# Performance work log

Hardware: AMD Instinct MI355X
Metric: run time of the kernel (lower is better)

The kernel has to match this reference:

```python
import jax, jax.numpy as jnp
import numpy as np

N = 100000
E = 1600000
IN_DIM = 128
HID = 64
NCOMM = 32


def setup_inputs() -> dict:
    key = jax.random.key(0)
    k = jax.random.split(key, 8)
    x = jax.random.normal(k[0], (N, IN_DIM), dtype=jnp.float32)
    edge_index = jax.random.randint(k[1], (2, E), 0, N, dtype=jnp.int64)
    s1 = 1.0 / np.sqrt(IN_DIM)
    s2 = 1.0 / np.sqrt(HID)
    W1 = jax.random.uniform(k[2], (IN_DIM, HID), jnp.float32, -s1, s1)
    b1 = jnp.zeros((HID,), jnp.float32)
    W2 = jax.random.uniform(k[3], (HID, HID), jnp.float32, -s2, s2)
    b2 = jnp.zeros((HID,), jnp.float32)
    Wfc = jax.random.uniform(k[4], (HID, NCOMM), jnp.float32, -s2, s2)
    bfc = jax.random.uniform(k[5], (NCOMM,), jnp.float32, -s2, s2)
    return {"x": x, "edge_index": edge_index, "W1": W1, "b1": b1,
            "W2": W2, "b2": b2, "Wfc": Wfc, "bfc": bfc}


def gcn_conv(x, row, col, norm, W, b):
    # PyG GCNConv: linear -> gather(source) * norm -> scatter_add(target) -> + bias
    h = x @ W                                    # [N, out]
    msgs = h[row] * norm[:, None]                # [E+N, out] gather (memory-bound)
    agg = jax.ops.segment_sum(msgs, col, num_segments=x.shape[0])
    return agg + b


def reference(x, edge_index, W1, b1, W2, b2, Wfc, bfc):
    n = x.shape[0]
    # add self-loops (PyG GCNConv default)
    loop = jnp.arange(n, dtype=edge_index.dtype)
    row = jnp.concatenate([edge_index[0], loop])  # source
    col = jnp.concatenate([edge_index[1], loop])  # target
    # symmetric normalization D^{-1/2} (A+I) D^{-1/2}
    deg = jax.ops.segment_sum(jnp.ones_like(col, dtype=x.dtype), col, num_segments=n)
    dinv = jnp.where(deg > 0, jax.lax.rsqrt(deg), 0.0)
    norm = dinv[row] * dinv[col]
    h = jax.nn.relu(gcn_conv(x, row, col, norm, W1, b1))   # dropout = identity (eval)
    h = jax.nn.relu(gcn_conv(h, row, col, norm, W2, b2))
    return jax.nn.sigmoid(h @ Wfc + bfc)
```

## Files before the change

kernel.cpp:

```cpp
#include <hip/hip_runtime.h>
#include <hip/hip_fp16.h>
#include <math.h>

#define N_NODES 100000
#define N_EDGES 1600000
#define IN_DIM  128
#define HID     64
#define NCOMM   32
#define NB        391
#define BSHIFT    8
#define BCAP      6144
#define EPB       4096
#define NBIN_BLK  391

typedef _Float16 f16x8 __attribute__((ext_vector_type(8)));
typedef float    f32x4 __attribute__((ext_vector_type(4)));

__global__ void k_detect(const unsigned int* __restrict__ e, int* __restrict__ flag) {
  int lane = threadIdx.x;
  unsigned v = 0;
  #pragma unroll
  for (int i = 0; i < 4; ++i) v |= e[2 * (lane * 4 + i) + 1];
  unsigned long long nz = __ballot(v != 0u);
  if (lane == 0) *flag = (nz == 0ull) ? 1 : 0;
}

__device__ __forceinline__ int load_idx(const int* e32, long long pos, int is64) {
  if (is64) return (int)(((const long long*)e32)[pos]);
  return e32[pos];
}

__global__ __launch_bounds__(256) void k_bin(const int* __restrict__ e, int* __restrict__ bcnt,
                                             unsigned* __restrict__ ebuf, const int* __restrict__ flag) {
  __shared__ int cnt[NB];
  __shared__ int base[NB];
  for (int i = threadIdx.x; i < NB; i += 256) cnt[i] = 0;
  __syncthreads();
  int is64 = *flag;
  long long eb = (long long)blockIdx.x * EPB;
  int rr[EPB / 256], cc[EPB / 256], lr[EPB / 256];
  #pragma unroll
  for (int j = 0; j < EPB / 256; ++j) {
    long long eid = eb + j * 256 + threadIdx.x;
    if (eid < N_EDGES) {
      rr[j] = load_idx(e, eid, is64);
      cc[j] = load_idx(e, (long long)N_EDGES + eid, is64);
      lr[j] = atomicAdd(&cnt[cc[j] >> BSHIFT], 1);
    }
  }
  __syncthreads();
  for (int b = threadIdx.x; b < NB; b += 256)
    base[b] = cnt[b] ? atomicAdd(&bcnt[b], cnt[b]) : 0;
  __syncthreads();
  #pragma unroll
  for (int j = 0; j < EPB / 256; ++j) {
    long long eid = eb + j * 256 + threadIdx.x;
    if (eid < N_EDGES) {
      int bb = cc[j] >> BSHIFT;
      int pos = bb * BCAP + base[bb] + lr[j];
      ebuf[pos] = ((unsigned)(cc[j] & 255) << 17) | (unsigned)rr[j];
    }
  }
}

__global__ __launch_bounds__(256) void k_degsort(const unsigned* __restrict__ ebuf, const int* __restrict__ bcnt,
                                                 float* __restrict__ dinv, int2* __restrict__ parr,
                                                 int* __restrict__ srow) {
  __shared__ int cnt[256];
  __shared__ int scn[256];
  __shared__ int cur[256];
  __shared__ unsigned eds[BCAP];
  int t = threadIdx.x;
  int b = blockIdx.x;
  int c0 = b << BSHIFT;
  int n = bcnt[b];
  cnt[t] = 0;
  __syncthreads();
  for (int i = t; i < n; i += 256) {
    unsigned w = ebuf[b * BCAP + i];
    eds[i] = w;
    atomicAdd(&cnt[w >> 17], 1);
  }
  __syncthreads();
  int d = cnt[t];
  scn[t] = d;
  __syncthreads();
  for (int off = 1; off < 256; off <<= 1) {
    int u = (t >= off) ? scn[t - off] : 0;
    __syncthreads();
    scn[t] += u;
    __syncthreads();
  }
  int sabs = b * BCAP + scn[t] - d;
  int node = c0 + t;
  if (node < N_NODES) {
    dinv[node] = rsqrtf((float)d + 1.0f);
    parr[node] = make_int2(sabs, sabs + d);
  }
  cur[t] = sabs;
  __syncthreads();
  for (int i = t; i < n; i += 256) {
    unsigned w = eds[i];
    int pos = atomicAdd(&cur[w >> 17], 1);
    srow[pos] = (int)(w & 0x1FFFFu);
  }
}

template<int K, int M, bool FINAL, bool INH>
__global__ __launch_bounds__(256) void k_mfma(const void* __restrict__ X, const float* __restrict__ W,
                                              void* __restrict__ Y, const float* __restrict__ bias,
                                              const float* __restrict__ dscale) {
  constexpr int NN = M / 16;
  constexpr int KS = K / 32;
  __shared__ char smem[M * K * 2];

  const int tid = threadIdx.x;
  for (int i = tid; i < K * M / 4; i += 256) {
    int k  = i / (M / 4);
    int mf = (i % (M / 4)) * 4;
    float4 wv = *(const float4*)(W + (size_t)k * M + mf);
    float wa[4] = {wv.x, wv.y, wv.z, wv.w};
    #pragma unroll
    for (int c = 0; c < 4; ++c) {
      int m = mf + c;
      int byte_off = m * (2 * K) + ((((k >> 3) << 4)) ^ ((m & 7) << 4)) + (k & 7) * 2;
      *(_Float16*)(smem + byte_off) = (_Float16)wa[c];
    }
  }
  __syncthreads();

  const int lane = tid & 63;
  const int wv_  = tid >> 6;
  const int rowbase = blockIdx.x * 128 + wv_ * 32;
  const int lr = lane & 15;
  const int kg = lane >> 4;
  const int r0 = rowbase + lr;
  const int r1 = r0 + 16;
  const int rc0 = (r0 < N_NODES) ? r0 : (N_NODES - 1);
  const int rc1 = (r1 < N_NODES) ? r1 : (N_NODES - 1);

  f32x4 acc[2][NN] = {};

  #pragma unroll
  for (int ks = 0; ks < KS; ++ks) {
    const int k0 = ks * 32 + kg * 8;
    f16x8 a0, a1;
    if constexpr (!INH) {
      const float* xr = (const float*)X;
      float4 u0 = *(const float4*)(xr + (size_t)rc0 * K + k0);
      float4 u1 = *(const float4*)(xr + (size_t)rc0 * K + k0 + 4);
      float4 u2 = *(const float4*)(xr + (size_t)rc1 * K + k0);
      float4 u3 = *(const float4*)(xr + (size_t)rc1 * K + k0 + 4);
      a0[0] = (_Float16)u0.x; a0[1] = (_Float16)u0.y; a0[2] = (_Float16)u0.z; a0[3] = (_Float16)u0.w;
      a0[4] = (_Float16)u1.x; a0[5] = (_Float16)u1.y; a0[6] = (_Float16)u1.z; a0[7] = (_Float16)u1.w;
      a1[0] = (_Float16)u2.x; a1[1] = (_Float16)u2.y; a1[2] = (_Float16)u2.z; a1[3] = (_Float16)u2.w;
      a1[4] = (_Float16)u3.x; a1[5] = (_Float16)u3.y; a1[6] = (_Float16)u3.z; a1[7] = (_Float16)u3.w;
    } else {
      const char* xb = (const char*)X;
      a0 = *(const f16x8*)(xb + (size_t)rc0 * (2 * K) + k0 * 2);
      a1 = *(const f16x8*)(xb + (size_t)rc1 * (2 * K) + k0 * 2);
    }
    const int slot = (k0 >> 3) << 4;
    #pragma unroll
    for (int n = 0; n < NN; ++n) {
      const int col = n * 16 + lr;
      f16x8 b = *(const f16x8*)(smem + col * (2 * K) + (slot ^ ((col & 7) << 4)));
      acc[0][n] = __builtin_amdgcn_mfma_f32_16x16x32_f16(a0, b, acc[0][n], 0, 0, 0);
      acc[1][n] = __builtin_amdgcn_mfma_f32_16x16x32_f16(a1, b, acc[1][n], 0, 0, 0);
    }
  }

  #pragma unroll
  for (int m2 = 0; m2 < 2; ++m2) {
    #pragma unroll
    for (int r = 0; r < 4; ++r) {
      const int row = rowbase + m2 * 16 + kg * 4 + r;
      if (row < N_NODES) {
        float ds = FINAL ? 0.f : dscale[row];
        #pragma unroll
        for (int n = 0; n < NN; ++n) {
          const int col = n * 16 + lr;
          float v = acc[m2][n][r];
          if constexpr (FINAL) {
            v += bias[col];
            v = 1.f / (1.f + __expf(-v));
            ((float*)Y)[(size_t)row * M + col] = v;
          } else {
            ((__half*)Y)[(size_t)row * M + col] = __float2half(v * ds);
          }
        }
      }
    }
  }
}

__device__ __forceinline__ void addrow(float* acc, uint4 h) {
  __half2 p0 = *(__half2*)&h.x;
  __half2 p1 = *(__half2*)&h.y;
  __half2 p2 = *(__half2*)&h.z;
  __half2 p3 = *(__half2*)&h.w;
  float2 f0 = __half22float2(p0);
  float2 f1 = __half22float2(p1);
  float2 f2 = __half22float2(p2);
  float2 f3 = __half22float2(p3);
  acc[0] += f0.x; acc[1] += f0.y;
  acc[2] += f1.x; acc[3] += f1.y;
  acc[4] += f2.x; acc[5] += f2.y;
  acc[6] += f3.x; acc[7] += f3.y;
}

__global__ __launch_bounds__(256) void k_agg(const __half* __restrict__ H, __half* __restrict__ O,
                                             const int2* __restrict__ parr, const int* __restrict__ srow,
                                             const float* __restrict__ dinv, const float* __restrict__ bias) {
  int wid  = (blockIdx.x * 256 + threadIdx.x) >> 6;
  int lane = threadIdx.x & 63;
  if (wid >= N_NODES) return;
  const int q  = lane >> 3;
  const int fl = lane & 7;
  const char* Hb = (const char*)H;
  int2 se = parr[wid];
  int s = se.x, e = se.y;
  float acc[8] = {0.f, 0.f, 0.f, 0.f, 0.f, 0.f, 0.f, 0.f};
  for (int j = s; j < e; j += 16) {
    int i0 = j + q;
    int i1 = j + 8 + q;
    int r0 = srow[i0];
    int r1 = srow[i1];
    r0 = (i0 < e) ? r0 : N_NODES;
    r1 = (i1 < e) ? r1 : N_NODES;
    uint4 h0 = *(const uint4*)(Hb + (size_t)((unsigned)r0 * 128u + (unsigned)fl * 16u));
    uint4 h1 = *(const uint4*)(Hb + (size_t)((unsigned)r1 * 128u + (unsigned)fl * 16u));
    addrow(acc, h0);
    addrow(acc, h1);
  }
  if (q == 0) {
    uint4 hb = *(const uint4*)(Hb + (size_t)((unsigned)wid * 128u + (unsigned)fl * 16u));
    addrow(acc, hb);
  }
  #pragma unroll
  for (int m = 8; m < 64; m <<= 1) {
    #pragma unroll
    for (int i = 0; i < 8; ++i) acc[i] += __shfl_xor(acc[i], m, 64);
  }
  if (lane < 8) {
    float di = dinv[wid];
    float4 ba = ((const float4*)bias)[2 * fl + 0];
    float4 bb = ((const float4*)bias)[2 * fl + 1];
    __half2 o0 = __floats2half2_rn(fmaxf(acc[0] * di + ba.x, 0.f), fmaxf(acc[1] * di + ba.y, 0.f));
    __half2 o1 = __floats2half2_rn(fmaxf(acc[2] * di + ba.z, 0.f), fmaxf(acc[3] * di + ba.w, 0.f));
    __half2 o2 = __floats2half2_rn(fmaxf(acc[4] * di + bb.x, 0.f), fmaxf(acc[5] * di + bb.y, 0.f));
    __half2 o3 = __floats2half2_rn(fmaxf(acc[6] * di + bb.z, 0.f), fmaxf(acc[7] * di + bb.w, 0.f));
    uint4 pv;
    pv.x = *(unsigned*)&o0;
    pv.y = *(unsigned*)&o1;
    pv.z = *(unsigned*)&o2;
    pv.w = *(unsigned*)&o3;
    *(uint4*)((char*)O + (size_t)wid * (HID * 2) + fl * 16) = pv;
  }
}

extern "C" void kernel_launch(void* const* d_in, const int* in_sizes, int n_in,
                              void* d_out, int out_size, void* d_ws, size_t ws_size,
                              hipStream_t stream) {
  const float* x   = (const float*)d_in[0];
  const int*   e   = (const int*)d_in[1];
  const float* W1  = (const float*)d_in[2];
  const float* b1  = (const float*)d_in[3];
  const float* W2  = (const float*)d_in[4];
  const float* b2  = (const float*)d_in[5];
  const float* Wfc = (const float*)d_in[6];
  const float* bfc = (const float*)d_in[7];
  float* out = (float*)d_out;

  char* ws = (char*)d_ws;
  __half*   hbuf = (__half*)  (ws);
  unsigned* ebuf = (unsigned*)(ws);
  int*      srow = (int*)     (ws + 12800192);
  __half*   abuf = (__half*)  (ws + 22409472);
  float*    dinv = (float*)   (ws + 35209472);
  int2*     parr = (int2*)    (ws + 35609472);
  int*      flag = (int*)     (ws + 36409472);
  int*      bcnt = (int*)     (ws + 36409536);

  hipMemsetAsync(bcnt, 0, NB * sizeof(int), stream);
  hipMemsetAsync(ws + (size_t)N_NODES * 128, 0, 128, stream);
  k_detect<<<1, 64, 0, stream>>>((const unsigned int*)e, flag);
  k_bin<<<NBIN_BLK, 256, 0, stream>>>(e, bcnt, ebuf, flag);
  k_degsort<<<NB, 256, 0, stream>>>(ebuf, bcnt, dinv, parr, srow);

  const int gBlocks = (N_NODES + 127) / 128;
  k_mfma<IN_DIM, HID, false, false><<<gBlocks, 256, 0, stream>>>(x, W1, hbuf, nullptr, dinv);
  k_agg<<<N_NODES * 64 / 256, 256, 0, stream>>>(hbuf, abuf, parr, srow, dinv, b1);
  k_mfma<HID, HID, false, true><<<gBlocks, 256, 0, stream>>>(abuf, W2, hbuf, nullptr, dinv);
  k_agg<<<N_NODES * 64 / 256, 256, 0, stream>>>(hbuf, abuf, parr, srow, dinv, b2);
  k_mfma<HID, NCOMM, true, true><<<gBlocks, 256, 0, stream>>>(abuf, Wfc, out, bfc, nullptr);
}
```

Measured before the change: 188.1 us.

## Merge preprocessing launches, detect index width in-block, widen binning and sort grids

Two memsets and the detect kernel are replaced by one small init kernel, and each binning block now detects the int64/int32 index width itself from the first 256 high words. Binning uses half the edges per block across twice as many blocks, and the degree/sort kernel runs 512 threads per block. The goal is to cut launch count and per-kernel latency in the preprocessing phase and to raise parallelism there, at the cost of redundant width detection in every block and doubled global atomic traffic on the bucket counters.

```diff
diff --git a/kernel.cpp b/kernel.cpp
--- a/kernel.cpp
+++ b/kernel.cpp
@@ -10,33 +10,34 @@
 #define NB        391
 #define BSHIFT    8
 #define BCAP      6144
-#define EPB       4096
-#define NBIN_BLK  391
+#define EPB       2048
+#define NBIN_BLK  782
 
 typedef _Float16 f16x8 __attribute__((ext_vector_type(8)));
 typedef float    f32x4 __attribute__((ext_vector_type(4)));
-
-__global__ void k_detect(const unsigned int* __restrict__ e, int* __restrict__ flag) {
-  int lane = threadIdx.x;
-  unsigned v = 0;
-  #pragma unroll
-  for (int i = 0; i < 4; ++i) v |= e[2 * (lane * 4 + i) + 1];
-  unsigned long long nz = __ballot(v != 0u);
-  if (lane == 0) *flag = (nz == 0ull) ? 1 : 0;
-}
 
 __device__ __forceinline__ int load_idx(const int* e32, long long pos, int is64) {
   if (is64) return (int)(((const long long*)e32)[pos]);
   return e32[pos];
 }
 
+__global__ __launch_bounds__(512) void k_init(int* __restrict__ bcnt, int* __restrict__ zrow) {
+  int t = threadIdx.x;
+  if (t < NB) bcnt[t] = 0;
+  if (t >= 480) zrow[t - 480] = 0;
+}
+
 __global__ __launch_bounds__(256) void k_bin(const int* __restrict__ e, int* __restrict__ bcnt,
-                                             unsigned* __restrict__ ebuf, const int* __restrict__ flag) {
+                                             unsigned* __restrict__ ebuf) {
   __shared__ int cnt[NB];
   __shared__ int base[NB];
+  __shared__ int s_hi;
+  if (threadIdx.x == 0) s_hi = 0;
   for (int i = threadIdx.x; i < NB; i += 256) cnt[i] = 0;
   __syncthreads();
-  int is64 = *flag;
+  if (((const unsigned*)e)[2 * threadIdx.x + 1] != 0u) atomicOr(&s_hi, 1);
+  __syncthreads();
+  const int is64 = (s_hi == 0);
   long long eb = (long long)blockIdx.x * EPB;
   int rr[EPB / 256], cc[EPB / 256], lr[EPB / 256];
   #pragma unroll
@@ -63,7 +64,7 @@
   }
 }
 
-__global__ __launch_bounds__(256) void k_degsort(const unsigned* __restrict__ ebuf, const int* __restrict__ bcnt,
+__global__ __launch_bounds__(512) void k_degsort(const unsigned* __restrict__ ebuf, const int* __restrict__ bcnt,
                                                  float* __restrict__ dinv, int2* __restrict__ parr,
                                                  int* __restrict__ srow) {
   __shared__ int cnt[256];
@@ -74,32 +75,34 @@
   int b = blockIdx.x;
   int c0 = b << BSHIFT;
   int n = bcnt[b];
-  cnt[t] = 0;
-  __syncthreads();
-  for (int i = t; i < n; i += 256) {
+  if (t < 256) cnt[t] = 0;
+  __syncthreads();
+  for (int i = t; i < n; i += 512) {
     unsigned w = ebuf[b * BCAP + i];
     eds[i] = w;
     atomicAdd(&cnt[w >> 17], 1);
   }
   __syncthreads();
-  int d = cnt[t];
-  scn[t] = d;
+  int d = (t < 256) ? cnt[t] : 0;
+  if (t < 256) scn[t] = d;
   __syncthreads();
   for (int off = 1; off < 256; off <<= 1) {
-    int u = (t >= off) ? scn[t - off] : 0;
+    int u = (t >= off && t < 256) ? scn[t - off] : 0;
     __syncthreads();
-    scn[t] += u;
+    if (t < 256) scn[t] += u;
     __syncthreads();
   }
-  int sabs = b * BCAP + scn[t] - d;
-  int node = c0 + t;
-  if (node < N_NODES) {
-    dinv[node] = rsqrtf((float)d + 1.0f);
-    parr[node] = make_int2(sabs, sabs + d);
-  }
-  cur[t] = sabs;
-  __syncthreads();
-  for (int i = t; i < n; i += 256) {
+  if (t < 256) {
+    int sabs = b * BCAP + scn[t] - d;
+    int node = c0 + t;
+    if (node < N_NODES) {
+      dinv[node] = rsqrtf((float)d + 1.0f);
+      parr[node] = make_int2(sabs, sabs + d);
+    }
+    cur[t] = sabs;
+  }
+  __syncthreads();
+  for (int i = t; i < n; i += 512) {
     unsigned w = eds[i];
     int pos = atomicAdd(&cur[w >> 17], 1);
     srow[pos] = (int)(w & 0x1FFFFu);
@@ -279,14 +282,11 @@
   __half*   abuf = (__half*)  (ws + 22409472);
   float*    dinv = (float*)   (ws + 35209472);
   int2*     parr = (int2*)    (ws + 35609472);
-  int*      flag = (int*)     (ws + 36409472);
   int*      bcnt = (int*)     (ws + 36409536);
 
-  hipMemsetAsync(bcnt, 0, NB * sizeof(int), stream);
-  hipMemsetAsync(ws + (size_t)N_NODES * 128, 0, 128, stream);
-  k_detect<<<1, 64, 0, stream>>>((const unsigned int*)e, flag);
-  k_bin<<<NBIN_BLK, 256, 0, stream>>>(e, bcnt, ebuf, flag);
-  k_degsort<<<NB, 256, 0, stream>>>(ebuf, bcnt, dinv, parr, srow);
+  k_init<<<1, 512, 0, stream>>>(bcnt, (int*)(ws + (size_t)N_NODES * 128));
+  k_bin<<<NBIN_BLK, 256, 0, stream>>>(e, bcnt, ebuf);
+  k_degsort<<<NB, 512, 0, stream>>>(ebuf, bcnt, dinv, parr, srow);
 
   const int gBlocks = (N_NODES + 127) / 128;
   k_mfma<IN_DIM, HID, false, false><<<gBlocks, 256, 0, stream>>>(x, W1, hbuf, nullptr, dinv);
```

New measurement: 187.1 us, median of 2. No clear change (-0.5%).
